# Optimization experiments

Measured on AMD Instinct MI355X. Metric: run time of the kernel, lower is better.

The kernel has to match this reference:

```python
import jax, jax.numpy as jnp
import numpy as np
from jax import lax

EPS = 1e-5
K = 16

def bn(x, g, b):
    # BatchNorm2d in training mode: biased batch stats over (B,H,W)
    m = x.mean(axis=(0, 2, 3), keepdims=True)
    v = x.var(axis=(0, 2, 3), keepdims=True)
    return (x - m) * lax.rsqrt(v + EPS) * g.reshape(1, -1, 1, 1) + b.reshape(1, -1, 1, 1)

def lrelu(x):
    return jnp.where(x >= 0, x, 0.01 * x)

def conv1x1(x, w, b):  # x:[B,C,N,K], w:[O,C]
    return jnp.einsum('bcnk,oc->bonk', x, w) + b.reshape(1, -1, 1, 1)

def edge_features_xyz(x, pc, k):
    B, C, N = x.shape
    xt = jnp.swapaxes(x, 1, 2)                      # [B,N,C]
    xs = jnp.sum(xt * xt, axis=2, keepdims=True)    # [B,N,1]
    dist = -2.0 * jnp.einsum('bnc,bcm->bnm', xt, x) + xs + jnp.swapaxes(xs, 1, 2)
    idx = jnp.argsort(dist, axis=2)[:, :, 1:k + 1]  # [B,N,k] skip self
    gather = jax.vmap(lambda fb, ib: fb[:, ib])     # [C,N],[N,k]->[C,N,k]
    nb = gather(x, idx)                             # [B,C,N,k]
    nb_xyz = gather(pc, idx)                        # [B,3,N,k]
    central = jnp.broadcast_to(x[..., None], (B, C, N, k))
    central_xyz = jnp.broadcast_to(pc[..., None], (B, 3, N, k))
    e_fea = jnp.concatenate([central, nb - central], axis=1)          # [B,2C,N,k]
    e_xyz = jnp.concatenate([central_xyz, nb_xyz - central_xyz], axis=1)  # [B,6,N,k]
    return e_fea, e_xyz

def forward(x, pc, fea_w, fea_b, fea_g, fea_be, xyz_w, xyz_b, xyz_g, xyz_be,
            all1_w, all1_b, all1_g, all1_be, all2_w, all2_b, all2_g, all2_be,
            inte_w, inte_b, inte_g, inte_be, c2_w, c2_b, c2_g, c2_be):
    B, Fin, N = x.shape
    k = K
    e_fea, e_xyz = edge_features_xyz(x, pc, k)      # [B,2Fin,N,k],[B,6,N,k]
    w_fea = lrelu(bn(conv1x1(e_fea, fea_w, fea_b), fea_g, fea_be))   # [B,16,N,k]
    w_xyz = lrelu(bn(conv1x1(e_xyz, xyz_w, xyz_b), xyz_g, xyz_be))   # [B,16,N,k]
    w = w_fea * w_xyz
    w = lrelu(bn(conv1x1(w, all1_w, all1_b), all1_g, all1_be))       # [B,64,N,k]
    w = lrelu(bn(conv1x1(w, all2_w, all2_b), all2_g, all2_be))       # [B,2Fin,N,k]
    w = jax.nn.softmax(w, axis=-1)
    CC = 2 * Fin
    # inte_conv_hk: Conv2d(2Fin->4Fin, kernel [1, k//2+1]) -> [B,4Fin,N,k//2]
    inte = lax.conv_general_dilated(e_fea, inte_w, (1, 1), 'VALID',
                                    dimension_numbers=('NCHW', 'OIHW', 'NCHW'))
    inte = inte + inte_b.reshape(1, -1, 1, 1)
    inte = lrelu(bn(inte, inte_g, inte_be))
    # torch reshape dance: [B,4Fin,N,k/2] -> [B,N,4Fin,k/2] -> [B,N,2Fin,2,k/2] -> [B,N,2Fin,k] -> [B,2Fin,N,k]
    inte = jnp.transpose(inte, (0, 2, 1, 3)).reshape(B, N, CC, 2, k // 2)
    inte = inte.reshape(B, N, CC, k).transpose(0, 2, 1, 3)
    inte_x = inte * w
    merge = jnp.concatenate([e_fea, inte_x], axis=3)                 # [B,2Fin,N,2k]
    # conv2: kernel [1,2k] spans full width -> contraction
    out = jnp.einsum('bcnw,ocw->bon', merge, c2_w[:, :, 0, :]) + c2_b.reshape(1, -1, 1)
    out = out[..., None]                                             # [B,2Fout,N,1]
    out = jnp.maximum(bn(out, c2_g, c2_be), 0.0)                     # ReLU
    Fout = out.shape[1] // 2
    return out.reshape(B, Fout, 2 * N)

def setup_inputs():
    B, Fin, Fout, N, k = 8, 64, 64, 2048, 16
    ks = jax.random.split(jax.random.key(0), 10)
    p = lambda i, s, sc=0.05: jax.random.normal(ks[i], s, jnp.float32) * sc
    return {
        'x': p(0, (B, Fin, N), 1.0),
        'pc': p(1, (B, 3, N), 1.0),
        'fea_w': p(2, (16, 2 * Fin)), 'fea_b': jnp.zeros(16), 'fea_g': jnp.ones(16), 'fea_be': jnp.zeros(16),
        'xyz_w': p(3, (16, 6)), 'xyz_b': jnp.zeros(16), 'xyz_g': jnp.ones(16), 'xyz_be': jnp.zeros(16),
        'all1_w': p(4, (64, 16)), 'all1_b': jnp.zeros(64), 'all1_g': jnp.ones(64), 'all1_be': jnp.zeros(64),
        'all2_w': p(5, (2 * Fin, 64)), 'all2_b': jnp.zeros(2 * Fin), 'all2_g': jnp.ones(2 * Fin), 'all2_be': jnp.zeros(2 * Fin),
        'inte_w': p(6, (4 * Fin, 2 * Fin, 1, k // 2 + 1)), 'inte_b': jnp.zeros(4 * Fin), 'inte_g': jnp.ones(4 * Fin), 'inte_be': jnp.zeros(4 * Fin),
        'c2_w': p(7, (2 * Fout, 2 * Fin, 1, 2 * k)), 'c2_b': jnp.zeros(2 * Fout), 'c2_g': jnp.ones(2 * Fout), 'c2_be': jnp.zeros(2 * Fout),
    }

def reference(x, pc, fea_w, fea_b, fea_g, fea_be, xyz_w, xyz_b, xyz_g, xyz_be,
              all1_w, all1_b, all1_g, all1_be, all2_w, all2_b, all2_g, all2_be,
              inte_w, inte_b, inte_g, inte_be, c2_w, c2_b, c2_g, c2_be):
    return forward(x, pc, fea_w, fea_b, fea_g, fea_be, xyz_w, xyz_b, xyz_g, xyz_be,
                   all1_w, all1_b, all1_g, all1_be, all2_w, all2_b, all2_g, all2_be,
                   inte_w, inte_b, inte_g, inte_be, c2_w, c2_b, c2_g, c2_be)
```

## Files before the change

kernel.cpp:

```cpp
#include <hip/hip_runtime.h>
#include <math.h>

typedef unsigned short ushort_t;

#define B_   8
#define N_   2048
#define K_   16
#define C2_  128
#define C4_  256
#define KH_  8
#define TAP_ 9
#define NK_  32768
#define EPSv 1e-5f
#define BIGF 3.0e38f
#define NMASK 2047

constexpr size_t AL(size_t x) { return (x + 255) & ~(size_t)255; }
constexpr size_t OFF_XT   = 0;
constexpr size_t OFF_IDX  = OFF_XT  + AL(4ull * B_ * N_ * 64);
constexpr size_t OFF_U1   = OFF_IDX + AL(4ull * B_ * N_ * K_);
constexpr size_t OFF_V1   = OFF_U1  + AL(4ull * B_ * 16 * N_);
constexpr size_t OFF_U2   = OFF_V1  + AL(4ull * B_ * N_ * 16);
constexpr size_t OFF_V2   = OFF_U2  + AL(4ull * B_ * 16 * N_);
constexpr size_t OFF_S    = OFF_V2  + AL(4ull * B_ * N_ * 16);
constexpr size_t OFF_P    = OFF_S   + AL(4ull * B_ * N_ * C2_);
constexpr size_t OFF_W1   = OFF_P   + AL(4ull * B_ * N_ * C4_);
constexpr size_t OFF_QB   = OFF_W1  + AL(4ull * B_ * 16 * NK_);
constexpr size_t OFF_ITB  = OFF_QB  + AL(2ull * (size_t)B_ * N_ * TAP_ * C4_);
constexpr size_t OFF_A4B  = OFF_ITB + AL(2ull * (size_t)B_ * N_ * 2048);
constexpr size_t OFF_M    = OFF_A4B + AL(2ull * (size_t)B_ * N_ * 2048);
constexpr size_t OFF_PART = OFF_M   + AL(2ull * (size_t)B_ * N_ * 2048);
constexpr size_t OFF_OUT2 = OFF_PART+ AL(4ull * 2 * (size_t)B_ * N_ * C2_);
constexpr size_t OFF_WQ2  = OFF_OUT2+ AL(4ull * B_ * N_ * C2_);
constexpr size_t OFF_WC2  = OFF_WQ2 + AL(4ull * TAP_ * C4_ * 64);
constexpr size_t OFF_WP2  = OFF_WC2 + AL(4ull * 3072 * C2_);
constexpr size_t OFF_WS2  = OFF_WP2 + AL(4ull * C4_ * 64);
constexpr size_t OFF_WU12 = OFF_WS2 + AL(4ull * C2_ * 64);
constexpr size_t OFF_WV12 = OFF_WU12+ AL(4ull * 16 * 64);
constexpr size_t OFF_WU22 = OFF_WV12+ AL(4ull * 16 * 64);
constexpr size_t OFF_WV22 = OFF_WU22+ AL(4ull * 64);
constexpr size_t OFF_A12  = OFF_WV22+ AL(4ull * 64);
constexpr size_t OFF_A22  = OFF_A12 + AL(4ull * 64 * 16);
constexpr size_t OFF_ST   = OFF_A22 + AL(4ull * C2_ * 64);
constexpr size_t OFF_PROG = OFF_ST  + AL(4ull * 4096);
constexpr size_t POOL_SZ  = OFF_PROG + AL(4ull * 64);

static char* g_pool_mem = nullptr;
struct PoolInit {
  PoolInit() { if (hipMalloc((void**)&g_pool_mem, POOL_SZ) != hipSuccess) g_pool_mem = nullptr; }
};
static PoolInit g_pool_init;

#define ST_S1S 0
#define ST_S1Q 16
#define ST_S2S 32
#define ST_S2Q 48
#define ST_S5S 64
#define ST_S5Q 320
#define ST_S4S 576
#define ST_S4Q 704
#define ST_S6S 832
#define ST_S6Q 960
#define ST_B1SC 1088
#define ST_B1SH 1104
#define ST_B2SC 1120
#define ST_B2SH 1136
#define ST_B3SC 1152
#define ST_B3SH 1216
#define ST_B4SC 1280
#define ST_B4SH 1408
#define ST_B5SC 1536
#define ST_B5SH 1792
#define ST_B6SC 2048
#define ST_B6SH 2176
#define ST_S3M  2304
#define ST_S3V  2440

#define BASE(b)  char* bb = (b)
#define P_XT   ((float*)(bb + OFF_XT))
#define P_IDX  ((int*)(bb + OFF_IDX))
#define P_U1   ((float*)(bb + OFF_U1))
#define P_V1   ((float*)(bb + OFF_V1))
#define P_U2   ((float*)(bb + OFF_U2))
#define P_V2   ((float*)(bb + OFF_V2))
#define P_Sb   ((float*)(bb + OFF_S))
#define P_P    ((float*)(bb + OFF_P))
#define P_W1   ((float*)(bb + OFF_W1))
#define P_QB   ((ushort_t*)(bb + OFF_QB))
#define P_IT   ((ushort_t*)(bb + OFF_ITB))
#define P_A4   ((ushort_t*)(bb + OFF_A4B))
#define P_M    ((ushort_t*)(bb + OFF_M))
#define P_PART ((float*)(bb + OFF_PART))
#define P_OUT2 ((float*)(bb + OFF_OUT2))
#define P_WQ2  ((float*)(bb + OFF_WQ2))
#define P_WC2  ((float*)(bb + OFF_WC2))
#define P_WP2  ((float*)(bb + OFF_WP2))
#define P_WS2  ((float*)(bb + OFF_WS2))
#define P_WU12 ((float*)(bb + OFF_WU12))
#define P_WV12 ((float*)(bb + OFF_WV12))
#define P_WU22 ((float*)(bb + OFF_WU22))
#define P_WV22 ((float*)(bb + OFF_WV22))
#define P_A12  ((float*)(bb + OFF_A12))
#define P_A22  ((float*)(bb + OFF_A22))
#define P_ST   ((float*)(bb + OFF_ST))
#define P_PROG ((int*)(bb + OFF_PROG))

#define PROG(id) do { if (threadIdx.x == 0) atomicAdd(&P_PROG[(id)], 1); } while (0)

static __device__ __forceinline__ float lrelu(float x) { return x >= 0.0f ? x : 0.01f * x; }
static __device__ __forceinline__ float bf2f(unsigned h) {
  union { float f; unsigned u; } v; v.u = h << 16; return v.f;
}
static __device__ __forceinline__ ushort_t f2bf(float f) {
  union { float f; unsigned u; } v; v.f = f;
  unsigned r = v.u + 0x7fffu + ((v.u >> 16) & 1u);
  return (ushort_t)(r >> 16);
}

__global__ __launch_bounds__(256) void zero_kernel(char* base)
{
  BASE(base);
  for (int i = threadIdx.x; i < 4096; i += 256) P_ST[i] = 0.0f;
  for (int i = threadIdx.x; i < 64; i += 256) P_PROG[i] = 0;
  __syncthreads();
  if (threadIdx.x == 0) P_PROG[0] = 1;
}

__global__ __launch_bounds__(256) void xt_kernel(char* base, const float* __restrict__ x)
{
  BASE(base);
  PROG(8);
  int b = blockIdx.x >> 5; int m0 = (blockIdx.x & 31) * 64;
  int t = threadIdx.x;
  __shared__ float tile[64 * 65];
  for (int i = t; i < 4096; i += 256) {
    int ml = i & 63, c = i >> 6;
    tile[c * 65 + ml] = x[((size_t)(b * 64 + c)) * N_ + m0 + ml];
  }
  __syncthreads();
  for (int i = t; i < 4096; i += 256) {
    int c = i & 63, ml = i >> 6;
    P_XT[((size_t)(b * N_) + m0 + ml) * 64 + c] = tile[c * 65 + ml];
  }
}

__global__ __launch_bounds__(256) void prep_kernel(char* base,
    const float* __restrict__ fea_w,
    const float* __restrict__ xyz_w, const float* __restrict__ inte_w,
    const float* __restrict__ c2_w, const float* __restrict__ all1_w,
    const float* __restrict__ all2_w)
{
  BASE(base);
  PROG(1);
  int i = blockIdx.x * 256 + threadIdx.x;
  if (i < 1024) { int o = i & 15, c = i >> 4;
    P_WU12[i] = fea_w[o * 128 + c] - fea_w[o * 128 + 64 + c]; return; }
  i -= 1024;
  if (i < 1024) { int o = i & 15, c = i >> 4;
    P_WV12[i] = fea_w[o * 128 + 64 + c]; return; }
  i -= 1024;
  if (i < 64) { int c = i & 3, o = i >> 2;
    P_WU22[i] = (c < 3) ? (xyz_w[o * 6 + c] - xyz_w[o * 6 + 3 + c]) : 0.0f; return; }
  i -= 64;
  if (i < 64) { int c = i & 3, o = i >> 2;
    P_WV22[i] = (c < 3) ? xyz_w[o * 6 + 3 + c] : 0.0f; return; }
  i -= 64;
  if (i < 16384) { int o = i & 255, c = i >> 8;
    float s = 0.0f;
    for (int t = 0; t < TAP_; t++)
      s += inte_w[(o * 128 + c) * TAP_ + t] - inte_w[(o * 128 + 64 + c) * TAP_ + t];
    P_WP2[i] = s; return; }
  i -= 16384;
  if (i < 147456) {
    int o = i & 255; int tc = i >> 8; int c = tc & 63; int tt = tc >> 6;
    P_WQ2[i] = inte_w[(o * 128 + 64 + c) * TAP_ + tt]; return; }
  i -= 147456;
  if (i < 8192) { int o = i & 127, c = i >> 7;
    float s = 0.0f;
    for (int p = 0; p < 16; p++)
      s += c2_w[(o * 128 + c) * 32 + p] - c2_w[(o * 128 + 64 + c) * 32 + p];
    P_WS2[i] = s; return; }
  i -= 8192;
  if (i < 393216) { int o = i & 127; int k = i >> 7; float v;
    if (k < 1024) { int c = k >> 4, p = k & 15; v = c2_w[(o * 128 + 64 + c) * 32 + p]; }
    else { int kr = k - 1024; int cc = kr >> 4, kk = kr & 15; v = c2_w[(o * 128 + cc) * 32 + 16 + kk]; }
    P_WC2[i] = v; return; }
  i -= 393216;
  if (i < 1024) { int c = i & 15, o = i >> 4; P_A12[i] = all1_w[o * 16 + c]; return; }
  i -= 1024;
  if (i < 8192) {
    int o = i & 127, c = i >> 7; P_A22[i] = all2_w[o * 64 + c]; return; }
}

__global__ __launch_bounds__(256) void phaseA_kernel(char* base,
                                                     const float* __restrict__ x,
                                                     const float* __restrict__ pc)
{
  BASE(base);
  PROG(2);
  __shared__ __align__(16) char smem[33824];
  int bid = blockIdx.x;
  int t = threadIdx.x;
  if (bid % 5 != 0) {
    int kb = bid - bid / 5 - 1;
    int b = kb >> 9; int n0 = (kb & 511) * 4;
    float (*sdist)[N_] = (float(*)[N_])smem;
    float (*xn)[64]    = (float(*)[64])(smem + 32768);
    float* sxn         = (float*)(smem + 32768 + 1024);
    {
      int nn = t >> 6, c = t & 63;
      xn[nn][c] = P_XT[((size_t)(b * N_) + n0 + nn) * 64 + c];
    }
    __syncthreads();
    if (t < 4) {
      float s = 0.0f;
      for (int c = 0; c < 64; c++) { float v = xn[t][c]; s += v * v; }
      sxn[t] = s;
    }
    __syncthreads();
    float dd[32]; float xs[8];
#pragma unroll
    for (int i = 0; i < 32; i++) dd[i] = 0.0f;
#pragma unroll
    for (int i = 0; i < 8; i++) xs[i] = 0.0f;
    const float* xbase = x + (size_t)b * 64 * N_ + (t << 3);
    for (int cq = 0; cq < 16; cq++) {
      float4 a0 = *(const float4*)&xn[0][cq * 4];
      float4 a1 = *(const float4*)&xn[1][cq * 4];
      float4 a2 = *(const float4*)&xn[2][cq * 4];
      float4 a3 = *(const float4*)&xn[3][cq * 4];
      float p[4][8];
#pragma unroll
      for (int cc = 0; cc < 4; cc++) {
        const float* xr = xbase + (size_t)(cq * 4 + cc) * N_;
        float4 u = *(const float4*)xr;
        float4 v = *(const float4*)(xr + 4);
        p[cc][0] = u.x; p[cc][1] = u.y; p[cc][2] = u.z; p[cc][3] = u.w;
        p[cc][4] = v.x; p[cc][5] = v.y; p[cc][6] = v.z; p[cc][7] = v.w;
      }
#pragma unroll
      for (int j = 0; j < 8; j++) {
        float x0 = p[0][j], x1 = p[1][j], x2 = p[2][j], x3 = p[3][j];
        xs[j] += x0 * x0 + x1 * x1 + x2 * x2 + x3 * x3;
        dd[0 * 8 + j] += a0.x * x0 + a0.y * x1 + a0.z * x2 + a0.w * x3;
        dd[1 * 8 + j] += a1.x * x0 + a1.y * x1 + a1.z * x2 + a1.w * x3;
        dd[2 * 8 + j] += a2.x * x0 + a2.y * x1 + a2.z * x2 + a2.w * x3;
        dd[3 * 8 + j] += a3.x * x0 + a3.y * x1 + a3.z * x2 + a3.w * x3;
      }
    }
    float sx0 = sxn[0], sx1 = sxn[1], sx2 = sxn[2], sx3 = sxn[3];
    int mb = t << 3;
#pragma unroll
    for (int j = 0; j < 8; j++) {
      int m = mb + j;
      float d0 = -2.0f * dd[0 * 8 + j] + sx0 + xs[j];
      float d1 = -2.0f * dd[1 * 8 + j] + sx1 + xs[j];
      float d2 = -2.0f * dd[2 * 8 + j] + sx2 + xs[j];
      float d3 = -2.0f * dd[3 * 8 + j] + sx3 + xs[j];
      sdist[0][m] = (m == n0 + 0) ? BIGF : d0;
      sdist[1][m] = (m == n0 + 1) ? BIGF : d1;
      sdist[2][m] = (m == n0 + 2) ? BIGF : d2;
      sdist[3][m] = (m == n0 + 3) ? BIGF : d3;
    }
    __syncthreads();
    int ln = t & 63; int wv = t >> 6;
    float v[32];
#pragma unroll
    for (int j = 0; j < 32; j++) v[j] = sdist[wv][ln + j * 64];
    float bv = v[0]; int bj = 0;
#pragma unroll
    for (int j = 1; j < 32; j++) { if (v[j] < bv) { bv = v[j]; bj = j; } }
    int* op = P_IDX + ((size_t)(b * N_) + n0 + wv) * K_;
    for (int it = 0; it < K_; it++) {
      float rv = bv; int ri = ln + (bj << 6);
#pragma unroll
      for (int off = 32; off > 0; off >>= 1) {
        float ov = __shfl_xor(rv, off);
        int oi = __shfl_xor(ri, off);
        if (ov < rv || (ov == rv && oi < ri)) { rv = ov; ri = oi; }
      }
      if (ln == 0) op[it] = ri;
      if ((ri & 63) == ln) {
        int slot = ri >> 6;
#pragma unroll
        for (int j = 0; j < 32; j++) v[j] = (j == slot) ? BIGF : v[j];
        bv = v[0]; bj = 0;
#pragma unroll
        for (int j = 1; j < 32; j++) { if (v[j] < bv) { bv = v[j]; bj = j; } }
      }
    }
    return;
  }
  int s = bid / 5;
  if (s < 512) {
    int b = s >> 6; int m0 = (s & 63) * 32;
    float (*actS)[40] = (float(*)[40])smem;
    float (*pcs)[32]  = (float(*)[32])(smem + 10240);
    for (int i = t; i < 2048; i += 256) {
      int c = i & 63, mm = i >> 6;
      actS[c][mm] = P_XT[((size_t)(b * N_) + m0 + mm) * 64 + c];
    }
    if (t < 96) {
      int c = t >> 5, mm = t & 31;
      pcs[c][mm] = pc[(b * 3 + c) * N_ + m0 + mm];
    }
    __syncthreads();
    size_t bN = (size_t)(b * N_);
    {
      int og = t & 31, pg = t >> 5;
      float acc[8][4];
#pragma unroll
      for (int oi = 0; oi < 8; oi++)
#pragma unroll
        for (int pj = 0; pj < 4; pj++) acc[oi][pj] = 0.0f;
      for (int c = 0; c < 64; c++) {
        float4 a = *(const float4*)&actS[c][pg * 4];
        const float* wr = P_WP2 + c * 256 + og * 8;
        float4 w0 = *(const float4*)wr;
        float4 w1 = *(const float4*)(wr + 4);
        float av[4] = {a.x, a.y, a.z, a.w};
        float wv[8] = {w0.x, w0.y, w0.z, w0.w, w1.x, w1.y, w1.z, w1.w};
#pragma unroll
        for (int oi = 0; oi < 8; oi++)
#pragma unroll
          for (int pj = 0; pj < 4; pj++) acc[oi][pj] += wv[oi] * av[pj];
      }
#pragma unroll
      for (int pj = 0; pj < 4; pj++) {
        float* pp = P_P + (bN + m0 + pg * 4 + pj) * C4_ + og * 8;
        *(float4*)pp = make_float4(acc[0][pj], acc[1][pj], acc[2][pj], acc[3][pj]);
        *(float4*)(pp + 4) = make_float4(acc[4][pj], acc[5][pj], acc[6][pj], acc[7][pj]);
      }
    }
    {
      int og = t & 15, pg = t >> 4;
      float acc[8][2];
#pragma unroll
      for (int oi = 0; oi < 8; oi++) { acc[oi][0] = 0.0f; acc[oi][1] = 0.0f; }
      for (int c = 0; c < 64; c++) {
        float a0 = actS[c][pg * 2], a1 = actS[c][pg * 2 + 1];
        const float* wr = P_WS2 + c * 128 + og * 8;
        float4 w0 = *(const float4*)wr;
        float4 w1 = *(const float4*)(wr + 4);
        float wv[8] = {w0.x, w0.y, w0.z, w0.w, w1.x, w1.y, w1.z, w1.w};
#pragma unroll
        for (int oi = 0; oi < 8; oi++) { acc[oi][0] += wv[oi] * a0; acc[oi][1] += wv[oi] * a1; }
      }
#pragma unroll
      for (int pj = 0; pj < 2; pj++) {
        float* sp = P_Sb + (bN + m0 + pg * 2 + pj) * C2_ + og * 8;
        *(float4*)sp = make_float4(acc[0][pj], acc[1][pj], acc[2][pj], acc[3][pj]);
        *(float4*)(sp + 4) = make_float4(acc[4][pj], acc[5][pj], acc[6][pj], acc[7][pj]);
      }
    }
    {
      int o = t & 15, pg = t >> 4;
      float aU[2] = {0.0f, 0.0f}, aV[2] = {0.0f, 0.0f};
      for (int c = 0; c < 64; c++) {
        float wu = P_WU12[c * 16 + o];
        float wv = P_WV12[c * 16 + o];
        float a0 = actS[c][pg * 2], a1 = actS[c][pg * 2 + 1];
        aU[0] += wu * a0; aU[1] += wu * a1;
        aV[0] += wv * a0; aV[1] += wv * a1;
      }
      float u0 = P_WU22[o * 4], u1 = P_WU22[o * 4 + 1], u2w = P_WU22[o * 4 + 2];
      float v0 = P_WV22[o * 4], v1 = P_WV22[o * 4 + 1], v2w = P_WV22[o * 4 + 2];
#pragma unroll
      for (int pj = 0; pj < 2; pj++) {
        int m = m0 + pg * 2 + pj;
        P_U1[((b * 16 + o) << 11) + m] = aU[pj];
        P_V1[(bN + m) * 16 + o] = aV[pj];
        float p0 = pcs[0][pg * 2 + pj], p1 = pcs[1][pg * 2 + pj], p2 = pcs[2][pg * 2 + pj];
        P_U2[((b * 16 + o) << 11) + m] = u0 * p0 + u1 * p1 + u2w * p2;
        P_V2[(bN + m) * 16 + o] = v0 * p0 + v1 * p1 + v2w * p2;
      }
    }
    return;
  }
  {
    int q = s - 512;
    int b = q >> 6; int m0 = (q & 63) * 32;
    float (*actS)[40] = (float(*)[40])smem;
    for (int i = t; i < 2048; i += 256) {
      int c = i & 63, mm = i >> 6;
      actS[c][mm] = P_XT[((size_t)(b * N_) + m0 + mm) * 64 + c];
    }
    __syncthreads();
    int og = t & 31;
    int pg = t >> 5;
    int m = m0 + pg * 4;
    for (int t9 = 0; t9 < TAP_; t9++) {
      const float* wbase = P_WQ2 + ((size_t)t9 * 64) * 256 + og * 8;
      float acc[8][4];
#pragma unroll
      for (int oi = 0; oi < 8; oi++)
#pragma unroll
        for (int pj = 0; pj < 4; pj++) acc[oi][pj] = 0.0f;
      for (int kc = 0; kc < 64; kc++) {
        float4 a = *(const float4*)&actS[kc][pg * 4];
        const float* wr = wbase + (size_t)kc * 256;
        float4 w0 = *(const float4*)wr;
        float4 w1 = *(const float4*)(wr + 4);
        float av[4] = {a.x, a.y, a.z, a.w};
        float wv[8] = {w0.x, w0.y, w0.z, w0.w, w1.x, w1.y, w1.z, w1.w};
#pragma unroll
        for (int oi = 0; oi < 8; oi++)
#pragma unroll
          for (int pj = 0; pj < 4; pj++)
            acc[oi][pj] += wv[oi] * av[pj];
      }
#pragma unroll
      for (int pj = 0; pj < 4; pj++) {
        ushort_t* qp = P_QB + ((size_t)(b * N_ + m + pj) * TAP_ + t9) * C4_ + og * 8;
        unsigned u0 = (unsigned)f2bf(acc[0][pj]) | ((unsigned)f2bf(acc[1][pj]) << 16);
        unsigned u1 = (unsigned)f2bf(acc[2][pj]) | ((unsigned)f2bf(acc[3][pj]) << 16);
        unsigned u2 = (unsigned)f2bf(acc[4][pj]) | ((unsigned)f2bf(acc[5][pj]) << 16);
        unsigned u3 = (unsigned)f2bf(acc[6][pj]) | ((unsigned)f2bf(acc[7][pj]) << 16);
        *(uint4*)qp = make_uint4(u0, u1, u2, u3);
      }
    }
    return;
  }
}

__global__ __launch_bounds__(256) void stats12_kernel(char* base,
    const float* __restrict__ fea_b, const float* __restrict__ xyz_b)
{
  BASE(base);
  PROG(4);
  int b = blockIdx.x >> 7; int n0 = (blockIdx.x & 127) * 16;
  int t = threadIdx.x; int o = t & 15; int kk = t >> 4;
  float fb = fea_b[o], xb = xyz_b[o];
  float s1 = 0, q1 = 0, s2 = 0, q2 = 0;
  for (int nn = 0; nn < 16; nn++) {
    int n = n0 + nn;
    int m = P_IDX[((b << 11) + n) * K_ + kk] & NMASK;
    float a1 = fb + P_U1[((b * 16 + o) << 11) + n] + P_V1[(((size_t)(b << 11) + m) << 4) + o];
    s1 += a1; q1 += a1 * a1;
    float a2 = xb + P_U2[((b * 16 + o) << 11) + n] + P_V2[(((size_t)(b << 11) + m) << 4) + o];
    s2 += a2; q2 += a2 * a2;
  }
  __shared__ float red[256];
  red[t] = s1; __syncthreads();
  if (t < 16) { float s = 0; for (int k2 = 0; k2 < 16; k2++) s += red[k2 * 16 + t]; atomicAdd(&P_ST[ST_S1S + t], s); }
  __syncthreads();
  red[t] = q1; __syncthreads();
  if (t < 16) { float s = 0; for (int k2 = 0; k2 < 16; k2++) s += red[k2 * 16 + t]; atomicAdd(&P_ST[ST_S1Q + t], s); }
  __syncthreads();
  red[t] = s2; __syncthreads();
  if (t < 16) { float s = 0; for (int k2 = 0; k2 < 16; k2++) s += red[k2 * 16 + t]; atomicAdd(&P_ST[ST_S2S + t], s); }
  __syncthreads();
  red[t] = q2; __syncthreads();
  if (t < 16) { float s = 0; for (int k2 = 0; k2 < 16; k2++) s += red[k2 * 16 + t]; atomicAdd(&P_ST[ST_S2Q + t], s); }
}

__global__ __launch_bounds__(256) void finalize_bn_kernel(char* base,
                                   const float* __restrict__ g,
                                   const float* __restrict__ be,
                                   int sum_off, int sq_off, int sc_off, int sh_off,
                                   int nch, float inv_cnt, int kid)
{
  BASE(base);
  PROG(kid);
  int i = threadIdx.x;
  if (i < nch) {
    float mu = P_ST[sum_off + i] * inv_cnt;
    float var = fmaxf(P_ST[sq_off + i] * inv_cnt - mu * mu, 0.0f);
    float s = g[i] * rsqrtf(var + EPSv);
    P_ST[sc_off + i] = s; P_ST[sh_off + i] = be[i] - mu * s;
  }
}

__global__ __launch_bounds__(256) void w1_kernel(char* base,
    const float* __restrict__ fea_b, const float* __restrict__ xyz_b)
{
  BASE(base);
  PROG(7);
  int b = blockIdx.x >> 7; int n0 = (blockIdx.x & 127) * 16;
  int t = threadIdx.x;
  __shared__ int sidx[16 * 16];
  __shared__ __align__(16) float ol[16 * 260];
  {
    int nl = t >> 4, k = t & 15;
    sidx[nl * 16 + k] = P_IDX[((size_t)((b << 11) + n0 + nl)) * 16 + k] & NMASK;
  }
  __syncthreads();
  int c = t >> 4; int nl = t & 15; int n = n0 + nl;
  float u1 = P_U1[((b * 16 + c) << 11) + n];
  float u2 = P_U2[((b * 16 + c) << 11) + n];
  float c1 = fea_b[c] + u1, c2v = xyz_b[c] + u2;
  float s1 = P_ST[ST_B1SC + c], h1 = P_ST[ST_B1SH + c];
  float s2 = P_ST[ST_B2SC + c], h2 = P_ST[ST_B2SH + c];
  float o16[16];
#pragma unroll
  for (int kk = 0; kk < 16; kk++) {
    int m = sidx[nl * 16 + kk];
    float a1 = c1 + P_V1[(((size_t)(b << 11) + m) << 4) + c];
    a1 = lrelu(a1 * s1 + h1);
    float a2 = c2v + P_V2[(((size_t)(b << 11) + m) << 4) + c];
    a2 = lrelu(a2 * s2 + h2);
    o16[kk] = a1 * a2;
  }
  float* wp = P_W1 + ((size_t)(b * 16 + c)) * NK_ + ((size_t)n << 4);
#pragma unroll
  for (int j = 0; j < 4; j++)
    *(float4*)(wp + j * 4) = make_float4(o16[4 * j], o16[4 * j + 1], o16[4 * j + 2], o16[4 * j + 3]);
  float* orow = ol + c * 260 + nl * 16;
#pragma unroll
  for (int j = 0; j < 4; j++)
    *(float4*)(orow + j * 4) = make_float4(o16[4 * j], o16[4 * j + 1], o16[4 * j + 2], o16[4 * j + 3]);
  __syncthreads();
  if (t < 136) {
    int cc1 = 0, rem = t;
    while (rem >= 16 - cc1) { rem -= 16 - cc1; cc1++; }
    int cc2 = cc1 + rem;
    const float* r1 = ol + cc1 * 260;
    const float* r2 = ol + cc2 * 260;
    float acc = 0.0f;
    for (int e = 0; e < 256; e += 4) {
      float4 xv = *(const float4*)(r1 + e);
      float4 yv = *(const float4*)(r2 + e);
      acc += xv.x * yv.x + xv.y * yv.y + xv.z * yv.z + xv.w * yv.w;
    }
    atomicAdd(&P_ST[ST_S3M + t], acc);
  } else if (t < 152) {
    const float* r = ol + (t - 136) * 260;
    float acc = 0.0f;
    for (int e = 0; e < 256; e += 4) {
      float4 xv = *(const float4*)(r + e);
      acc += xv.x + xv.y + xv.z + xv.w;
    }
    atomicAdd(&P_ST[ST_S3V + t - 136], acc);
  }
}

__global__ __launch_bounds__(256) void finalize_bn3_kernel(char* base,
                                    const float* __restrict__ b1,
                                    const float* __restrict__ g,
                                    const float* __restrict__ be)
{
  BASE(base);
  PROG(9);
  int o = threadIdx.x;
  if (o >= 64) return;
  float A[16];
  for (int c = 0; c < 16; c++) A[c] = P_A12[o * 16 + c];
  float dv = 0.0f;
  for (int c = 0; c < 16; c++) dv += A[c] * P_ST[ST_S3V + c];
  float quad = 0.0f; int p = 0;
  for (int c1 = 0; c1 < 16; c1++)
    for (int c2 = c1; c2 < 16; c2++) {
      float m = P_ST[ST_S3M + p]; p++;
      quad += (c1 == c2 ? 1.0f : 2.0f) * A[c1] * A[c2] * m;
    }
  float bo = b1[o];
  const float inv = 1.0f / 262144.0f;
  float mean = dv * inv + bo;
  float e2 = quad * inv + 2.0f * bo * dv * inv + bo * bo;
  float var = fmaxf(e2 - mean * mean, 0.0f);
  float s = g[o] * rsqrtf(var + EPSv);
  P_ST[ST_B3SC + o] = s; P_ST[ST_B3SH + o] = be[o] - mean * s;
}

__global__ __launch_bounds__(256) void a4_kernel(char* base,
                                                 const float* __restrict__ all1_b,
                                                 const float* __restrict__ all2_b)
{
  BASE(base);
  PROG(10);
  int b = blockIdx.x >> 9; int col0 = (blockIdx.x & 511) * 64;
  int t = threadIdx.x;
  __shared__ float sw[16 * 68];
  __shared__ __align__(16) float hS[64 * 68];
  for (int i = t; i < 1024; i += 256) {
    int c = i >> 6, l = i & 63;
    sw[c * 68 + l] = P_W1[((size_t)(b * 16 + c)) * NK_ + col0 + l];
  }
  __syncthreads();
  {
    int col = t & 63; int q = t >> 6;
    float in16[16];
#pragma unroll
    for (int c = 0; c < 16; c++) in16[c] = sw[c * 68 + col];
    for (int oo = 0; oo < 16; oo++) {
      int o = q * 16 + oo;
      const float* wr = P_A12 + o * 16;
      float a = all1_b[o];
#pragma unroll
      for (int c = 0; c < 16; c++) a += wr[c] * in16[c];
      hS[o * 68 + col] = lrelu(a * P_ST[ST_B3SC + o] + P_ST[ST_B3SH + o]);
    }
  }
  __syncthreads();
  int cg = t & 15;
  int og = t >> 4;
  float acc[8][4];
#pragma unroll
  for (int oi = 0; oi < 8; oi++) {
    float bo = all2_b[og * 8 + oi];
#pragma unroll
    for (int cj = 0; cj < 4; cj++) acc[oi][cj] = bo;
  }
  for (int hk = 0; hk < 64; hk++) {
    float4 hv = *(const float4*)&hS[hk * 68 + cg * 4];
    const float* wr = P_A22 + hk * 128 + og * 8;
    float4 w0 = *(const float4*)wr;
    float4 w1 = *(const float4*)(wr + 4);
    float av[4] = {hv.x, hv.y, hv.z, hv.w};
    float wv[8] = {w0.x, w0.y, w0.z, w0.w, w1.x, w1.y, w1.z, w1.w};
#pragma unroll
    for (int oi = 0; oi < 8; oi++)
#pragma unroll
      for (int cj = 0; cj < 4; cj++)
        acc[oi][cj] += wv[oi] * av[cj];
  }
  int colb = col0 + cg * 4;
  int n = colb >> 4; int kk0 = colb & 15;
  ushort_t* dst = P_A4 + ((size_t)(b * N_) + n) * 2048 + kk0;
  float psum[8], qsum[8];
#pragma unroll
  for (int oi = 0; oi < 8; oi++) {
    int o = og * 8 + oi;
    unsigned lo = (unsigned)f2bf(acc[oi][0]) | ((unsigned)f2bf(acc[oi][1]) << 16);
    unsigned hi = (unsigned)f2bf(acc[oi][2]) | ((unsigned)f2bf(acc[oi][3]) << 16);
    *(uint2*)(dst + o * 16) = make_uint2(lo, hi);
    float r0 = bf2f(lo & 0xffffu), r1 = bf2f(lo >> 16);
    float r2 = bf2f(hi & 0xffffu), r3 = bf2f(hi >> 16);
    psum[oi] = r0 + r1 + r2 + r3;
    qsum[oi] = r0 * r0 + r1 * r1 + r2 * r2 + r3 * r3;
  }
  __syncthreads();
  float* redS = hS;
#pragma unroll
  for (int oi = 0; oi < 8; oi++) redS[(og * 8 + oi) * 16 + cg] = psum[oi];
  __syncthreads();
  if (t < 128) {
    float s = 0.0f;
    for (int j = 0; j < 16; j++) s += redS[t * 16 + j];
    atomicAdd(&P_ST[ST_S4S + t], s);
  }
  __syncthreads();
#pragma unroll
  for (int oi = 0; oi < 8; oi++) redS[(og * 8 + oi) * 16 + cg] = qsum[oi];
  __syncthreads();
  if (t < 128) {
    float s = 0.0f;
    for (int j = 0; j < 16; j++) s += redS[t * 16 + j];
    atomicAdd(&P_ST[ST_S4Q + t], s);
  }
}

__global__ __launch_bounds__(256) void softfuse_kernel(char* base)
{
  BASE(base);
  PROG(13);
  int rid = blockIdx.x * 256 + threadIdx.x;
  int cc = rid & 127; int r = rid >> 7;
  float s = P_ST[ST_B4SC + cc], h = P_ST[ST_B4SH + cc];
  size_t base_off = (size_t)r * 2048 + cc * 16;
  const ushort_t* pa = P_A4 + base_off;
  uint4 u0 = *(const uint4*)pa;
  uint4 u1 = *(const uint4*)(pa + 8);
  unsigned ws[8] = {u0.x, u0.y, u0.z, u0.w, u1.x, u1.y, u1.z, u1.w};
  float v[16];
#pragma unroll
  for (int j = 0; j < 8; j++) {
    union { float f; unsigned u; } lo, hi;
    lo.u = ws[j] << 16; hi.u = ws[j] & 0xffff0000u;
    v[2 * j] = lo.f; v[2 * j + 1] = hi.f;
  }
  float mx = -BIGF;
#pragma unroll
  for (int i = 0; i < 16; i++) {
    float y = lrelu(v[i] * s + h);
    v[i] = y; mx = fmaxf(mx, y);
  }
  float sum = 0.0f;
#pragma unroll
  for (int i = 0; i < 16; i++) { float e = expf(v[i] - mx); v[i] = e; sum += e; }
  float inv = (sum > 0.0f) ? 1.0f / sum : 0.0f;
#pragma unroll
  for (int i = 0; i < 16; i++) v[i] = bf2f((unsigned)f2bf(v[i] * inv));
  float s5a = P_ST[ST_B5SC + cc * 2],     h5a = P_ST[ST_B5SH + cc * 2];
  float s5b = P_ST[ST_B5SC + cc * 2 + 1], h5b = P_ST[ST_B5SH + cc * 2 + 1];
  const ushort_t* itp = P_IT + base_off;
  uint4 i0 = *(const uint4*)itp;
  uint4 i1 = *(const uint4*)(itp + 8);
  unsigned iw[8] = {i0.x, i0.y, i0.z, i0.w, i1.x, i1.y, i1.z, i1.w};
  unsigned mw[8];
#pragma unroll
  for (int j = 0; j < 8; j++) {
    union { float f; unsigned u; } il, ih;
    il.u = iw[j] << 16; ih.u = iw[j] & 0xffff0000u;
    float s5 = (j < 4) ? s5a : s5b;
    float h5 = (j < 4) ? h5a : h5b;
    float m0 = lrelu(il.f * s5 + h5) * v[2 * j];
    float m1 = lrelu(ih.f * s5 + h5) * v[2 * j + 1];
    mw[j] = (unsigned)f2bf(m0) | ((unsigned)f2bf(m1) << 16);
  }
  ushort_t* mp = P_M + base_off;
  *(uint4*)mp = make_uint4(mw[0], mw[1], mw[2], mw[3]);
  *(uint4*)(mp + 8) = make_uint4(mw[4], mw[5], mw[6], mw[7]);
}

__global__ __launch_bounds__(256) void inte_fused_kernel(char* base,
                                                         const float* __restrict__ inte_b)
{
  BASE(base);
  PROG(15);
  int b = blockIdx.x >> 9; int n0 = (blockIdx.x & 511) * 4;
  int t = threadIdx.x; int o = t;
  __shared__ int sidx[4][16];
  if (t < 64) sidx[t >> 4][t & 15] = P_IDX[((size_t)(b * N_) + n0 + (t >> 4)) * K_ + (t & 15)] & NMASK;
  __syncthreads();
  float bias = inte_b[o];
  float ssum = 0.0f, ssq = 0.0f;
  for (int nn = 0; nn < 4; nn++) {
    int n = n0 + nn;
    float bse = bias + P_P[((size_t)(b * N_) + n) * C4_ + o];
    float acc[8];
#pragma unroll
    for (int j = 0; j < 8; j++) acc[j] = bse;
    for (int p = 0; p < 16; p++) {
      const ushort_t* qr = P_QB + (size_t)(b * N_ + sidx[nn][p]) * TAP_ * C4_ + o;
#pragma unroll
      for (int tt = 0; tt < TAP_; tt++) {
        int j = p - tt;
        if (j >= 0 && j < 8) acc[j] += bf2f(((unsigned)qr[tt * C4_]) << 16 >> 16 << 16 >> 16);
      }
    }
    ushort_t* ip = P_IT + ((size_t)(b * N_) + n) * 2048 + o * 8;
#pragma unroll
    for (int j = 0; j < 8; j++) { float v = acc[j]; ip[j] = f2bf(v); ssum += v; ssq += v * v; }
  }
  atomicAdd(&P_ST[ST_S5S + o], ssum);
  atomicAdd(&P_ST[ST_S5Q + o], ssq);
}

__global__ __launch_bounds__(256) void final_conv_kernel(char* base)
{
  BASE(base);
  PROG(17);
  int ks = blockIdx.x & 1;
  int tile = (blockIdx.x >> 1) & 31; int b = blockIdx.x >> 6;
  int n0 = tile * 64;
  int t = threadIdx.x;
  int cg4 = (t & 15) * 4;
  int obase = (t >> 4) * 8;
  __shared__ __align__(16) float tileS[128 * 68];
  __shared__ int sidxT[16 * 64];
  for (int i = t; i < 1024; i += 256) {
    int cl = i & 63, p = i >> 6;
    sidxT[p * 64 + cl] = P_IDX[((size_t)(b * N_) + n0 + cl) * K_ + p] & NMASK;
  }
  float acc[32];
#pragma unroll
  for (int i = 0; i < 32; i++) acc[i] = 0.0f;
  int kbeg = ks * 1536;
  for (int k0 = kbeg; k0 < kbeg + 1536; k0 += 128) {
    __syncthreads();
    if (k0 < 1024) {
      int c0 = k0 >> 4;
      int cl = t & 63; int pg = t >> 6;
      for (int pp = 0; pp < 4; pp++) {
        int p = pg * 4 + pp;
        int m = sidxT[p * 64 + cl];
        const float* xp = P_XT + ((size_t)(b * N_) + m) * 64 + c0;
        float4 v0 = *(const float4*)xp;
        float4 v1 = *(const float4*)(xp + 4);
        tileS[(0 * 16 + p) * 68 + cl] = v0.x;
        tileS[(1 * 16 + p) * 68 + cl] = v0.y;
        tileS[(2 * 16 + p) * 68 + cl] = v0.z;
        tileS[(3 * 16 + p) * 68 + cl] = v0.w;
        tileS[(4 * 16 + p) * 68 + cl] = v1.x;
        tileS[(5 * 16 + p) * 68 + cl] = v1.y;
        tileS[(6 * 16 + p) * 68 + cl] = v1.z;
        tileS[(7 * 16 + p) * 68 + cl] = v1.w;
      }
    } else {
      int cl = t & 63; int kg = t >> 6;
      size_t rb = ((size_t)(b * N_) + n0 + cl) * 2048 + (size_t)(k0 - 1024) + kg * 32;
      const ushort_t* mp = P_M + rb;
      for (int j8 = 0; j8 < 4; j8++) {
        uint4 u = *(const uint4*)(mp + j8 * 8);
        unsigned ws[4] = {u.x, u.y, u.z, u.w};
#pragma unroll
        for (int q = 0; q < 4; q++) {
          union { float f; unsigned uu; } lo, hi;
          lo.uu = ws[q] << 16; hi.uu = ws[q] & 0xffff0000u;
          int kc = kg * 32 + j8 * 8 + q * 2;
          tileS[kc * 68 + cl] = lo.f;
          tileS[(kc + 1) * 68 + cl] = hi.f;
        }
      }
    }
    __syncthreads();
    for (int kc = 0; kc < 128; kc++) {
      float4 a = *(const float4*)&tileS[kc * 68 + cg4];
      const float* wr = P_WC2 + (size_t)(k0 + kc) * C2_ + obase;
      float4 w0 = *(const float4*)wr;
      float4 w1 = *(const float4*)(wr + 4);
      float av[4] = {a.x, a.y, a.z, a.w};
      float wv[8] = {w0.x, w0.y, w0.z, w0.w, w1.x, w1.y, w1.z, w1.w};
#pragma unroll
      for (int oi = 0; oi < 8; oi++)
#pragma unroll
        for (int cj = 0; cj < 4; cj++)
          acc[oi * 4 + cj] += wv[oi] * av[cj];
    }
  }
#pragma unroll
  for (int cj = 0; cj < 4; cj++) {
    float* op = P_PART + ((size_t)ks * B_ * N_ + (size_t)b * N_ + n0 + cg4 + cj) * C2_ + obase;
    *(float4*)op = make_float4(acc[0 * 4 + cj], acc[1 * 4 + cj], acc[2 * 4 + cj], acc[3 * 4 + cj]);
    *(float4*)(op + 4) = make_float4(acc[4 * 4 + cj], acc[5 * 4 + cj], acc[6 * 4 + cj], acc[7 * 4 + cj]);
  }
}

__global__ __launch_bounds__(256) void reduce_stats_kernel(char* base,
                                                           const float* __restrict__ c2_b)
{
  BASE(base);
  PROG(18);
  int r0 = blockIdx.x * 32;
  int t = threadIdx.x; int o = t & 127; int h = t >> 7;
  const size_t STRIDE = (size_t)B_ * N_ * C2_;
  float cb = c2_b[o];
  float s = 0, q = 0;
  for (int r = r0 + h; r < r0 + 32; r += 2) {
    size_t off = (size_t)r * C2_ + o;
    float v = cb + P_Sb[off] + P_PART[off] + P_PART[STRIDE + off];
    P_OUT2[off] = v;
    s += v; q += v * v;
  }
  __shared__ float rs[256], rq[256];
  rs[t] = s; rq[t] = q; __syncthreads();
  if (t < 128) {
    atomicAdd(&P_ST[ST_S6S + o], rs[t] + rs[t + 128]);
    atomicAdd(&P_ST[ST_S6Q + o], rq[t] + rq[t + 128]);
  }
}

__global__ __launch_bounds__(256) void output_kernel(char* base, float* __restrict__ out)
{
  BASE(base);
  PROG(20);
  int b = blockIdx.x >> 6; int n0 = (blockIdx.x & 63) * 32;
  int t = threadIdx.x;
  __shared__ float tile[32 * 133];
  for (int i = t; i < 4096; i += 256) {
    int o = i & 127, nl = i >> 7;
    float v = P_OUT2[((size_t)(b * N_) + n0 + nl) * C2_ + o];
    v = v * P_ST[ST_B6SC + o] + P_ST[ST_B6SH + o];
    tile[nl * 133 + o] = fmaxf(v, 0.0f);
  }
  __syncthreads();
  for (int i = t; i < 4096; i += 256) {
    int nl = i & 31, o = i >> 5;
    out[(((size_t)b * 64 + (o >> 1)) * 2 + (o & 1)) * 2048 + n0 + nl] = tile[nl * 133 + o];
  }
}

__global__ void diag_kernel(char* base, float* __restrict__ out)
{
  BASE(base);
  const int expctd[22] = {1, 2253, 5120, 0, 1024, 1, 1, 1024, 256, 1, 4096,
                          0, 1, 8192, 0, 4096, 1, 512, 512, 1, 512, 0};
  int t = threadIdx.x;
  int bad = 99;
  if (t < 22 && P_PROG[t] != expctd[t]) bad = t;
#pragma unroll
  for (int off = 32; off > 0; off >>= 1) {
    int ob = __shfl_xor(bad, off);
    if (ob < bad) bad = ob;
  }
  if (t == 0 && bad != 99) out[0] = 100.0f + 10.0f * (float)bad;
}

__global__ void code_kernel(float* __restrict__ out, float code)
{
  if (threadIdx.x == 0 && blockIdx.x == 0) out[0] = code;
}

extern "C" void kernel_launch(void* const* d_in, const int* in_sizes, int n_in,
                              void* d_out, int out_size, void* d_ws, size_t ws_size,
                              hipStream_t stream) {
  const float* x      = (const float*)d_in[0];
  const float* pc     = (const float*)d_in[1];
  const float* fea_w  = (const float*)d_in[2];
  const float* fea_b  = (const float*)d_in[3];
  const float* fea_g  = (const float*)d_in[4];
  const float* fea_be = (const float*)d_in[5];
  const float* xyz_w  = (const float*)d_in[6];
  const float* xyz_b  = (const float*)d_in[7];
  const float* xyz_g  = (const float*)d_in[8];
  const float* xyz_be = (const float*)d_in[9];
  const float* all1_w = (const float*)d_in[10];
  const float* all1_b = (const float*)d_in[11];
  const float* all1_g = (const float*)d_in[12];
  const float* all1_be= (const float*)d_in[13];
  const float* all2_w = (const float*)d_in[14];
  const float* all2_b = (const float*)d_in[15];
  const float* all2_g = (const float*)d_in[16];
  const float* all2_be= (const float*)d_in[17];
  const float* inte_w = (const float*)d_in[18];
  const float* inte_b = (const float*)d_in[19];
  const float* inte_g = (const float*)d_in[20];
  const float* inte_be= (const float*)d_in[21];
  const float* c2_w   = (const float*)d_in[22];
  const float* c2_b   = (const float*)d_in[23];
  const float* c2_g   = (const float*)d_in[24];
  const float* c2_be  = (const float*)d_in[25];
  float* out = (float*)d_out;
  (void)in_sizes; (void)n_in; (void)out_size; (void)d_ws; (void)ws_size;

  if (g_pool_mem == nullptr) {
    code_kernel<<<1, 64, 0, stream>>>(out, 500.0f);
    return;
  }
  char* base = g_pool_mem;

  zero_kernel<<<1, 256, 0, stream>>>(base);
  xt_kernel<<<256, 256, 0, stream>>>(base, x);
  prep_kernel<<<2253, 256, 0, stream>>>(base, fea_w, xyz_w, inte_w, c2_w, all1_w, all2_w);
  phaseA_kernel<<<5120, 256, 0, stream>>>(base, x, pc);
  stats12_kernel<<<1024, 256, 0, stream>>>(base, fea_b, xyz_b);
  finalize_bn_kernel<<<1, 256, 0, stream>>>(base, fea_g, fea_be, ST_S1S, ST_S1Q, ST_B1SC, ST_B1SH, 16, 1.0f / 262144.0f, 5);
  finalize_bn_kernel<<<1, 256, 0, stream>>>(base, xyz_g, xyz_be, ST_S2S, ST_S2Q, ST_B2SC, ST_B2SH, 16, 1.0f / 262144.0f, 6);
  w1_kernel<<<1024, 256, 0, stream>>>(base, fea_b, xyz_b);
  finalize_bn3_kernel<<<1, 256, 0, stream>>>(base, all1_b, all1_g, all1_be);
  a4_kernel<<<4096, 256, 0, stream>>>(base, all1_b, all2_b);
  finalize_bn_kernel<<<1, 256, 0, stream>>>(base, all2_g, all2_be, ST_S4S, ST_S4Q, ST_B4SC, ST_B4SH, 128, 1.0f / 262144.0f, 12);
  inte_fused_kernel<<<4096, 256, 0, stream>>>(base, inte_b);
  finalize_bn_kernel<<<1, 256, 0, stream>>>(base, inte_g, inte_be, ST_S5S, ST_S5Q, ST_B5SC, ST_B5SH, 256, 1.0f / 131072.0f, 16);
  softfuse_kernel<<<8192, 256, 0, stream>>>(base);
  final_conv_kernel<<<512, 256, 0, stream>>>(base);
  reduce_stats_kernel<<<512, 256, 0, stream>>>(base, c2_b);
  finalize_bn_kernel<<<1, 256, 0, stream>>>(base, c2_g, c2_be, ST_S6S, ST_S6Q, ST_B6SC, ST_B6SH, 128, 1.0f / 16384.0f, 19);
  output_kernel<<<512, 256, 0, stream>>>(base, out);
  diag_kernel<<<1, 64, 0, stream>>>(base, out);
}
```

Before: 1.193 ms.

## Merge stats12 and inte conv into one launch via block-index partitioning

Folds the BN1/BN2 statistics kernel and the inte convolution kernel into a single phaseB launch, interleaving block roles (every fifth block does stats work). The inte conv and its BN finalize are moved earlier in the stream, since they depend only on phaseA outputs. The aim is to remove a launch and its tail, and to let the light stats blocks overlap with the heavier gather-conv blocks. Both roles now share a 1 KB shared buffer, and the diagnostic progress counts are updated to match.

```diff
diff --git a/kernel.cpp b/kernel.cpp
--- a/kernel.cpp
+++ b/kernel.cpp
@@ -423,35 +423,75 @@
   }
 }
 
-__global__ __launch_bounds__(256) void stats12_kernel(char* base,
-    const float* __restrict__ fea_b, const float* __restrict__ xyz_b)
-{
-  BASE(base);
-  PROG(4);
-  int b = blockIdx.x >> 7; int n0 = (blockIdx.x & 127) * 16;
-  int t = threadIdx.x; int o = t & 15; int kk = t >> 4;
-  float fb = fea_b[o], xb = xyz_b[o];
-  float s1 = 0, q1 = 0, s2 = 0, q2 = 0;
-  for (int nn = 0; nn < 16; nn++) {
-    int n = n0 + nn;
-    int m = P_IDX[((b << 11) + n) * K_ + kk] & NMASK;
-    float a1 = fb + P_U1[((b * 16 + o) << 11) + n] + P_V1[(((size_t)(b << 11) + m) << 4) + o];
-    s1 += a1; q1 += a1 * a1;
-    float a2 = xb + P_U2[((b * 16 + o) << 11) + n] + P_V2[(((size_t)(b << 11) + m) << 4) + o];
-    s2 += a2; q2 += a2 * a2;
-  }
-  __shared__ float red[256];
-  red[t] = s1; __syncthreads();
-  if (t < 16) { float s = 0; for (int k2 = 0; k2 < 16; k2++) s += red[k2 * 16 + t]; atomicAdd(&P_ST[ST_S1S + t], s); }
-  __syncthreads();
-  red[t] = q1; __syncthreads();
-  if (t < 16) { float s = 0; for (int k2 = 0; k2 < 16; k2++) s += red[k2 * 16 + t]; atomicAdd(&P_ST[ST_S1Q + t], s); }
-  __syncthreads();
-  red[t] = s2; __syncthreads();
-  if (t < 16) { float s = 0; for (int k2 = 0; k2 < 16; k2++) s += red[k2 * 16 + t]; atomicAdd(&P_ST[ST_S2S + t], s); }
-  __syncthreads();
-  red[t] = q2; __syncthreads();
-  if (t < 16) { float s = 0; for (int k2 = 0; k2 < 16; k2++) s += red[k2 * 16 + t]; atomicAdd(&P_ST[ST_S2Q + t], s); }
+__global__ __launch_bounds__(256) void phaseB_kernel(char* base,
+                                                     const float* __restrict__ inte_b,
+                                                     const float* __restrict__ fea_b,
+                                                     const float* __restrict__ xyz_b)
+{
+  BASE(base);
+  PROG(15);
+  __shared__ __align__(16) char smem[1024];
+  int bid = blockIdx.x;
+  int t = threadIdx.x;
+  if (bid % 5 != 0) {
+    int kb = bid - bid / 5 - 1;
+    int b = kb >> 9; int n0 = (kb & 511) * 4;
+    int o = t;
+    int (*sidx)[16] = (int(*)[16])smem;
+    if (t < 64) sidx[t >> 4][t & 15] = P_IDX[((size_t)(b * N_) + n0 + (t >> 4)) * K_ + (t & 15)] & NMASK;
+    __syncthreads();
+    float bias = inte_b[o];
+    float ssum = 0.0f, ssq = 0.0f;
+    for (int nn = 0; nn < 4; nn++) {
+      int n = n0 + nn;
+      float bse = bias + P_P[((size_t)(b * N_) + n) * C4_ + o];
+      float acc[8];
+#pragma unroll
+      for (int j = 0; j < 8; j++) acc[j] = bse;
+      for (int p = 0; p < 16; p++) {
+        const ushort_t* qr = P_QB + (size_t)(b * N_ + sidx[nn][p]) * TAP_ * C4_ + o;
+#pragma unroll
+        for (int tt = 0; tt < TAP_; tt++) {
+          int j = p - tt;
+          if (j >= 0 && j < 8) acc[j] += bf2f(((unsigned)qr[tt * C4_]) << 16 >> 16 << 16 >> 16);
+        }
+      }
+      ushort_t* ip = P_IT + ((size_t)(b * N_) + n) * 2048 + o * 8;
+#pragma unroll
+      for (int j = 0; j < 8; j++) { float v = acc[j]; ip[j] = f2bf(v); ssum += v; ssq += v * v; }
+    }
+    atomicAdd(&P_ST[ST_S5S + o], ssum);
+    atomicAdd(&P_ST[ST_S5Q + o], ssq);
+    return;
+  }
+  {
+    int s = bid / 5;
+    int b = s >> 7; int n0 = (s & 127) * 16;
+    int o = t & 15; int kk = t >> 4;
+    float* red = (float*)smem;
+    float fb = fea_b[o], xb = xyz_b[o];
+    float s1 = 0, q1 = 0, s2 = 0, q2 = 0;
+    for (int nn = 0; nn < 16; nn++) {
+      int n = n0 + nn;
+      int m = P_IDX[((b << 11) + n) * K_ + kk] & NMASK;
+      float a1 = fb + P_U1[((b * 16 + o) << 11) + n] + P_V1[(((size_t)(b << 11) + m) << 4) + o];
+      s1 += a1; q1 += a1 * a1;
+      float a2 = xb + P_U2[((b * 16 + o) << 11) + n] + P_V2[(((size_t)(b << 11) + m) << 4) + o];
+      s2 += a2; q2 += a2 * a2;
+    }
+    red[t] = s1; __syncthreads();
+    if (t < 16) { float s = 0; for (int k2 = 0; k2 < 16; k2++) s += red[k2 * 16 + t]; atomicAdd(&P_ST[ST_S1S + t], s); }
+    __syncthreads();
+    red[t] = q1; __syncthreads();
+    if (t < 16) { float s = 0; for (int k2 = 0; k2 < 16; k2++) s += red[k2 * 16 + t]; atomicAdd(&P_ST[ST_S1Q + t], s); }
+    __syncthreads();
+    red[t] = s2; __syncthreads();
+    if (t < 16) { float s = 0; for (int k2 = 0; k2 < 16; k2++) s += red[k2 * 16 + t]; atomicAdd(&P_ST[ST_S2S + t], s); }
+    __syncthreads();
+    red[t] = q2; __syncthreads();
+    if (t < 16) { float s = 0; for (int k2 = 0; k2 < 16; k2++) s += red[k2 * 16 + t]; atomicAdd(&P_ST[ST_S2Q + t], s); }
+    return;
+  }
 }
 
 __global__ __launch_bounds__(256) void finalize_bn_kernel(char* base,
@@ -701,40 +741,6 @@
   ushort_t* mp = P_M + base_off;
   *(uint4*)mp = make_uint4(mw[0], mw[1], mw[2], mw[3]);
   *(uint4*)(mp + 8) = make_uint4(mw[4], mw[5], mw[6], mw[7]);
-}
-
-__global__ __launch_bounds__(256) void inte_fused_kernel(char* base,
-                                                         const float* __restrict__ inte_b)
-{
-  BASE(base);
-  PROG(15);
-  int b = blockIdx.x >> 9; int n0 = (blockIdx.x & 511) * 4;
-  int t = threadIdx.x; int o = t;
-  __shared__ int sidx[4][16];
-  if (t < 64) sidx[t >> 4][t & 15] = P_IDX[((size_t)(b * N_) + n0 + (t >> 4)) * K_ + (t & 15)] & NMASK;
-  __syncthreads();
-  float bias = inte_b[o];
-  float ssum = 0.0f, ssq = 0.0f;
-  for (int nn = 0; nn < 4; nn++) {
-    int n = n0 + nn;
-    float bse = bias + P_P[((size_t)(b * N_) + n) * C4_ + o];
-    float acc[8];
-#pragma unroll
-    for (int j = 0; j < 8; j++) acc[j] = bse;
-    for (int p = 0; p < 16; p++) {
-      const ushort_t* qr = P_QB + (size_t)(b * N_ + sidx[nn][p]) * TAP_ * C4_ + o;
-#pragma unroll
-      for (int tt = 0; tt < TAP_; tt++) {
-        int j = p - tt;
-        if (j >= 0 && j < 8) acc[j] += bf2f(((unsigned)qr[tt * C4_]) << 16 >> 16 << 16 >> 16);
-      }
-    }
-    ushort_t* ip = P_IT + ((size_t)(b * N_) + n) * 2048 + o * 8;
-#pragma unroll
-    for (int j = 0; j < 8; j++) { float v = acc[j]; ip[j] = f2bf(v); ssum += v; ssq += v * v; }
-  }
-  atomicAdd(&P_ST[ST_S5S + o], ssum);
-  atomicAdd(&P_ST[ST_S5Q + o], ssq);
 }
 
 __global__ __launch_bounds__(256) void final_conv_kernel(char* base)
@@ -864,8 +870,8 @@
 __global__ void diag_kernel(char* base, float* __restrict__ out)
 {
   BASE(base);
-  const int expctd[22] = {1, 2253, 5120, 0, 1024, 1, 1, 1024, 256, 1, 4096,
-                          0, 1, 8192, 0, 4096, 1, 512, 512, 1, 512, 0};
+  const int expctd[22] = {1, 2253, 5120, 0, 0, 1, 1, 1024, 256, 1, 4096,
+                          0, 1, 8192, 0, 5120, 1, 512, 512, 1, 512, 0};
   int t = threadIdx.x;
   int bad = 99;
   if (t < 22 && P_PROG[t] != expctd[t]) bad = t;
@@ -924,15 +930,14 @@
   xt_kernel<<<256, 256, 0, stream>>>(base, x);
   prep_kernel<<<2253, 256, 0, stream>>>(base, fea_w, xyz_w, inte_w, c2_w, all1_w, all2_w);
   phaseA_kernel<<<5120, 256, 0, stream>>>(base, x, pc);
-  stats12_kernel<<<1024, 256, 0, stream>>>(base, fea_b, xyz_b);
+  phaseB_kernel<<<5120, 256, 0, stream>>>(base, inte_b, fea_b, xyz_b);
   finalize_bn_kernel<<<1, 256, 0, stream>>>(base, fea_g, fea_be, ST_S1S, ST_S1Q, ST_B1SC, ST_B1SH, 16, 1.0f / 262144.0f, 5);
   finalize_bn_kernel<<<1, 256, 0, stream>>>(base, xyz_g, xyz_be, ST_S2S, ST_S2Q, ST_B2SC, ST_B2SH, 16, 1.0f / 262144.0f, 6);
+  finalize_bn_kernel<<<1, 256, 0, stream>>>(base, inte_g, inte_be, ST_S5S, ST_S5Q, ST_B5SC, ST_B5SH, 256, 1.0f / 131072.0f, 16);
   w1_kernel<<<1024, 256, 0, stream>>>(base, fea_b, xyz_b);
   finalize_bn3_kernel<<<1, 256, 0, stream>>>(base, all1_b, all1_g, all1_be);
   a4_kernel<<<4096, 256, 0, stream>>>(base, all1_b, all2_b);
   finalize_bn_kernel<<<1, 256, 0, stream>>>(base, all2_g, all2_be, ST_S4S, ST_S4Q, ST_B4SC, ST_B4SH, 128, 1.0f / 262144.0f, 12);
-  inte_fused_kernel<<<4096, 256, 0, stream>>>(base, inte_b);
-  finalize_bn_kernel<<<1, 256, 0, stream>>>(base, inte_g, inte_be, ST_S5S, ST_S5Q, ST_B5SC, ST_B5SH, 256, 1.0f / 131072.0f, 16);
   softfuse_kernel<<<8192, 256, 0, stream>>>(base);
   final_conv_kernel<<<512, 256, 0, stream>>>(base);
   reduce_stats_kernel<<<512, 256, 0, stream>>>(base, c2_b);
```

Measured after the change: 1.160 ms (median of 2 runs). 1.03x faster.
